# Kernel tuning notes

Measured on AMD Instinct MI355X. Metric: run time of the kernel, lower is better.

## Reference

```python
import jax, jax.numpy as jnp
import numpy as np

B, C, O, H, W, K, PAD = 8, 256, 256, 56, 56, 3, 1
KK = K * K


def setup_inputs() -> dict:
    key = jax.random.key(0)
    k1, k2, k3, k4 = jax.random.split(key, 4)
    x = jax.random.normal(k1, (B, C, H, W), jnp.float32)
    # offset conv params (original zero-inits; small random used so sampling is off-grid)
    w_off = jax.random.normal(k2, (2 * KK, C, K, K), jnp.float32) * 0.01
    b_off = jnp.zeros((2 * KK,), jnp.float32)
    # deformable conv weight/bias (torchvision DeformConv2d default has bias)
    w_dcn = jax.random.normal(k3, (O, C, K, K), jnp.float32) * (1.0 / np.sqrt(C * KK))
    b_dcn = jax.random.normal(k4, (O,), jnp.float32) * 0.01
    return dict(x=x, w_off=w_off, b_off=b_off, w_dcn=w_dcn, b_dcn=b_dcn)


def _conv3x3(x, w, b):
    y = jax.lax.conv_general_dilated(
        x, w, window_strides=(1, 1), padding=((PAD, PAD), (PAD, PAD)),
        dimension_numbers=('NCHW', 'OIHW', 'NCHW'))
    return y + b[None, :, None, None]


def _deform_sample(x, py, px):
    """Zero-padded bilinear gather of x[B,C,H,W] at (py,px)[B,KK,H,W] -> [B,C,KK,H,W]."""
    xf = x.reshape(B, C, H * W)
    y0 = jnp.floor(py)
    x0 = jnp.floor(px)
    fy = py - y0
    fx = px - x0
    val = 0.0
    for dy, dx, wgt in ((0, 0, (1 - fy) * (1 - fx)),
                        (0, 1, (1 - fy) * fx),
                        (1, 0, fy * (1 - fx)),
                        (1, 1, fy * fx)):
        yc = y0 + dy
        xc = x0 + dx
        ok = (yc >= 0) & (yc < H) & (xc >= 0) & (xc < W)  # zero-padding outside
        yi = jnp.clip(yc, 0, H - 1).astype(jnp.int32)
        xi = jnp.clip(xc, 0, W - 1).astype(jnp.int32)
        idx = (yi * W + xi).reshape(B, 1, KK * H * W)  # broadcast over channel dim
        g = jnp.take_along_axis(xf, idx, axis=2).reshape(B, C, KK, H, W)
        val = val + (wgt * ok)[:, None] * g
    return val


def reference(x, w_off, b_off, w_dcn, b_dcn):
    # 1) predict per-pixel offsets: [B, 2*K*K, H, W], torchvision layout (dy,dx) pairs
    off = _conv3x3(x, w_off, b_off)
    dy = off[:, 0::2]  # [B, KK, H, W]
    dx = off[:, 1::2]
    # 2) sampling grid: base pixel + kernel tap offset + learned offset
    ky = (jnp.arange(KK) // K - PAD).astype(jnp.float32)
    kx = (jnp.arange(KK) % K - PAD).astype(jnp.float32)
    hgrid = jnp.arange(H, dtype=jnp.float32)
    wgrid = jnp.arange(W, dtype=jnp.float32)
    py = hgrid[None, None, :, None] + ky[None, :, None, None] + dy
    px = wgrid[None, None, None, :] + kx[None, :, None, None] + dx
    # 3) bilinear gather + weighted accumulation over (c, kernel tap)
    val = _deform_sample(x, py, px)  # [B, C, KK, H, W]
    out = jnp.einsum('bckhw,ock->bohw', val, w_dcn.reshape(O, C, KK))
    return out + b_dcn[None, :, None, None]
```

## Files before the change

### kernel.cpp

```cpp
#include <hip/hip_runtime.h>

#define B_  8
#define C_  256
#define O_  256
#define H_  56
#define W_  56
#define HW_ 3136
#define KK_ 9
#define CK_ 2304
#define NKC 72

typedef __bf16    bf16x8 __attribute__((ext_vector_type(8)));
typedef float     f32x4  __attribute__((ext_vector_type(4)));

__device__ __forceinline__ void async16(const void* gsrc_lane, void* lds_uniform) {
    __builtin_amdgcn_global_load_lds(
        (const __attribute__((address_space(1))) unsigned int*)gsrc_lane,
        (__attribute__((address_space(3))) unsigned int*)lds_uniform, 16, 0, 0);
}

__device__ __forceinline__ int swz4(int r) { return (r & 3) ^ ((r >> 2) & 3); }

__device__ __forceinline__ float blo(unsigned u) {
    return __builtin_bit_cast(float, u << 16);
}
__device__ __forceinline__ float bhi(unsigned u) {
    return __builtin_bit_cast(float, u & 0xffff0000u);
}
__device__ __forceinline__ unsigned pkbf(float lo, float hi) {
    unsigned short a = __builtin_bit_cast(unsigned short, (__bf16)lo);
    unsigned short b = __builtin_bit_cast(unsigned short, (__bf16)hi);
    return (unsigned)a | ((unsigned)b << 16);
}

__device__ __forceinline__ uint4 bilin4(uint4 c00, uint4 c01, uint4 c10, uint4 c11,
                                        float4 wg) {
    uint4 o;
    float lo_, hi_;
    lo_ = wg.x*blo(c00.x) + wg.y*blo(c01.x) + wg.z*blo(c10.x) + wg.w*blo(c11.x);
    hi_ = wg.x*bhi(c00.x) + wg.y*bhi(c01.x) + wg.z*bhi(c10.x) + wg.w*bhi(c11.x);
    o.x = pkbf(lo_, hi_);
    lo_ = wg.x*blo(c00.y) + wg.y*blo(c01.y) + wg.z*blo(c10.y) + wg.w*blo(c11.y);
    hi_ = wg.x*bhi(c00.y) + wg.y*bhi(c01.y) + wg.z*bhi(c10.y) + wg.w*bhi(c11.y);
    o.y = pkbf(lo_, hi_);
    lo_ = wg.x*blo(c00.z) + wg.y*blo(c01.z) + wg.z*blo(c10.z) + wg.w*blo(c11.z);
    hi_ = wg.x*bhi(c00.z) + wg.y*bhi(c01.z) + wg.z*bhi(c10.z) + wg.w*bhi(c11.z);
    o.z = pkbf(lo_, hi_);
    lo_ = wg.x*blo(c00.w) + wg.y*blo(c01.w) + wg.z*blo(c10.w) + wg.w*blo(c11.w);
    hi_ = wg.x*bhi(c00.w) + wg.y*bhi(c01.w) + wg.z*bhi(c10.w) + wg.w*bhi(c11.w);
    o.w = pkbf(lo_, hi_);
    return o;
}

__global__ __launch_bounds__(256) void k_buildA(const float* __restrict__ w,
                                                unsigned short* __restrict__ wA) {
    int d  = blockIdx.x * 256 + threadIdx.x;
    int kc = d >> 13;
    int rd = d & 8191;
    int m  = rd >> 5;
    int pos = rd & 31;
    int q  = (pos >> 3) ^ swz4(m);
    int kl = q * 8 + (pos & 7);
    int gk = kc * 32 + kl;
    int tap = gk >> 8, c = gk & 255;
    __bf16 v = (__bf16)w[m * CK_ + c * KK_ + tap];
    wA[d] = __builtin_bit_cast(unsigned short, v);
}

__global__ __launch_bounds__(256) void k_transx(const float* __restrict__ x,
                                                unsigned short* __restrict__ xT) {
    __shared__ float s[64][65];
    int bt   = blockIdx.x;
    int c64  = bt & 3;
    int hw64 = (bt >> 2) % 49;
    int b    = bt / 196;
    int tx = threadIdx.x & 63;
    int ty = threadIdx.x >> 6;
#pragma unroll
    for (int i = 0; i < 16; ++i)
        s[i * 4 + ty][tx] =
            x[((size_t)(b * 256 + c64 * 64 + i * 4 + ty)) * HW_ + hw64 * 64 + tx];
    __syncthreads();
#pragma unroll
    for (int i = 0; i < 16; ++i) {
        float v = s[tx][i * 4 + ty];
        xT[((size_t)b * HW_ + hw64 * 64 + i * 4 + ty) * 256 + c64 * 64 + tx] =
            __builtin_bit_cast(unsigned short, (__bf16)v);
    }
}

__global__ __launch_bounds__(512) void k_offc1(const float* __restrict__ x,
                                               const float* __restrict__ w_off,
                                               float* __restrict__ part) {
    __shared__ float partial[8][64][18];
    int t  = threadIdx.x;
    int p  = t & 63;
    int cg = __builtin_amdgcn_readfirstlane(t >> 6);
    int blk  = blockIdx.x;
    int sl   = blk & 3;
    int un   = blk >> 2;
    int b    = un / 49;
    int pos0 = (un % 49) * 64;
    int pos  = pos0 + p;
    int h = pos / W_;
    int w = pos % W_;
    const float* xb = x + (size_t)b * C_ * HW_;

    float acc[18];
#pragma unroll
    for (int i = 0; i < 18; ++i) acc[i] = 0.f;

    for (int cc = 0; cc < 8; ++cc) {
        int c = sl * 64 + cg * 8 + cc;
        const float* xp = xb + c * HW_;
        float v[9];
#pragma unroll
        for (int dh = -1; dh <= 1; ++dh)
#pragma unroll
            for (int dw = -1; dw <= 1; ++dw) {
                int hh = h + dh, ww = w + dw;
                bool ok = (hh >= 0) & (hh < H_) & (ww >= 0) & (ww < W_);
                v[(dh + 1) * 3 + dw + 1] = ok ? xp[hh * W_ + ww] : 0.f;
            }
        const float* wc = w_off + c * KK_;
#pragma unroll
        for (int oc = 0; oc < 18; ++oc) {
            const float* wr = wc + oc * CK_;
#pragma unroll
            for (int k = 0; k < KK_; ++k)
                acc[oc] = fmaf(v[k], wr[k], acc[oc]);
        }
    }
#pragma unroll
    for (int oc = 0; oc < 18; ++oc) partial[cg][p][oc] = acc[oc];
    __syncthreads();

    float* po = part + (size_t)sl * (B_ * 18 * HW_);
    for (int e = t; e < 64 * 18; e += 512) {
        int oc = e >> 6;
        int pp = e & 63;
        float s = 0.f;
#pragma unroll
        for (int g = 0; g < 8; ++g) s += partial[g][pp][oc];
        po[((size_t)b * 18 + oc) * HW_ + pos0 + pp] = s;
    }
}

__global__ __launch_bounds__(256) void k_offc2(const float* __restrict__ part,
                                               const float* __restrict__ b_off,
                                               float* __restrict__ off) {
    int i = blockIdx.x * 256 + threadIdx.x;
    const int NP = B_ * 18 * HW_;
    int oc = (i / HW_) % 18;
    off[i] = part[i] + part[i + NP] + part[i + 2 * NP] + part[i + 3 * NP]
           + b_off[oc];
}

__device__ __forceinline__ void fstage(
    int s, int chNext, bool issueA, bool prod, bool reload,
    const char* xb, const char* gA0,
    __bf16 (*s_a)[8192], __bf16 (*s_b)[2048],
    int (*s_id)[64][4], float (*s_w)[64][4],
    int4& id, float4& wg,
    int n, int tc, int sc, int wv, int lid, int quad, int swz, int lo,
    f32x4 (&acc)[4][4]) {

    if (reload) {
        int tp1 = (s + 1) >> 3;
        id = *(const int4*)s_id[tp1][n];
        wg = *(const float4*)s_w[tp1][n];
    }
    uint4 c00, c01, c10, c11;
    if (prod) {
        const char* p = xb + chNext * 64 + tc * 16;
        c00 = *(const uint4*)(p + id.x);
        c01 = *(const uint4*)(p + id.y);
        c10 = *(const uint4*)(p + id.z);
        c11 = *(const uint4*)(p + id.w);
    }
    if (issueA) {
        const char* ga = gA0 + (size_t)(s + 2) * 16384;
        char* la = (char*)s_a[(s + 2) % 3];
#pragma unroll
        for (int j = 0; j < 4; ++j)
            async16(ga + wv * 4096 + j * 1024 + lo, la + wv * 4096 + j * 1024);
    }
    asm volatile("s_waitcnt vmcnt(12)" ::: "memory");

    const bf16x8* pa = (const bf16x8*)s_a[s % 3];
    const bf16x8* pb = (const bf16x8*)s_b[s & 1];
    bf16x8 af[4], bv[4];
#pragma unroll
    for (int mi = 0; mi < 4; ++mi)
        af[mi] = pa[(wv * 64 + mi * 16 + lid) * 4 + (quad ^ swz)];
#pragma unroll
    for (int ni = 0; ni < 4; ++ni)
        bv[ni] = pb[(ni * 16 + lid) * 4 + (quad ^ swz)];

    __builtin_amdgcn_s_setprio(1);
#pragma unroll
    for (int mi = 0; mi < 4; ++mi)
#pragma unroll
        for (int ni = 0; ni < 4; ++ni)
            acc[mi][ni] = __builtin_amdgcn_mfma_f32_16x16x32_bf16(
                af[mi], bv[ni], acc[mi][ni], 0, 0, 0);
    __builtin_amdgcn_s_setprio(0);

    if (prod) {
        uint4 o = bilin4(c00, c01, c10, c11, wg);
        *(uint4*)((char*)s_b[(s & 1) ^ 1] + n * 64 + sc * 16) = o;
    }
    asm volatile("s_waitcnt lgkmcnt(0)" ::: "memory");
    __builtin_amdgcn_s_barrier();
    __builtin_amdgcn_sched_barrier(0);
}

__global__ __launch_bounds__(256, 2) void k_fused(
    const unsigned short* __restrict__ xT,
    const float* __restrict__ off,
    const __bf16* __restrict__ wA,
    const float* __restrict__ b_dcn,
    float* __restrict__ out) {

    __shared__ __bf16 s_a[3][8192];
    __shared__ __bf16 s_b[2][2048];
    __shared__ int    s_id[KK_][64][4];
    __shared__ float  s_w [KK_][64][4];

    int g    = blockIdx.x;
    int b    = g / 49;
    int pos0 = (g % 49) * 64;
    int t    = threadIdx.x;
    int lane = t & 63;
    int wv   = t >> 6;
    int lid  = lane & 15;
    int quad = lane >> 4;
    int swz  = swz4(lid);

    for (int e = t; e < KK_ * 64; e += 256) {
        int k = e >> 6, n = e & 63;
        int pos = pos0 + n;
        int h = pos / W_, w = pos % W_;
        float dy = off[((size_t)b * 18 + 2 * k) * HW_ + pos];
        float dx = off[((size_t)b * 18 + 2 * k + 1) * HW_ + pos];
        float py = (float)(h + k / 3 - 1) + dy;
        float px = (float)(w + k % 3 - 1) + dx;
        float y0f = floorf(py), x0f = floorf(px);
        float fy = py - y0f, fx = px - x0f;
        int y0 = (int)y0f, x0 = (int)x0f;
        int y1 = y0 + 1,   x1 = x0 + 1;
        float oy0 = (y0 >= 0 && y0 < H_) ? 1.f : 0.f;
        float oy1 = (y1 >= 0 && y1 < H_) ? 1.f : 0.f;
        float ox0 = (x0 >= 0 && x0 < W_) ? 1.f : 0.f;
        float ox1 = (x1 >= 0 && x1 < W_) ? 1.f : 0.f;
        int y0c = min(max(y0, 0), H_ - 1), y1c = min(max(y1, 0), H_ - 1);
        int x0c = min(max(x0, 0), W_ - 1), x1c = min(max(x1, 0), W_ - 1);
        s_id[k][n][0] = (y0c * W_ + x0c) * 512;
        s_id[k][n][1] = (y0c * W_ + x1c) * 512;
        s_id[k][n][2] = (y1c * W_ + x0c) * 512;
        s_id[k][n][3] = (y1c * W_ + x1c) * 512;
        s_w[k][n][0] = (1.f - fy) * (1.f - fx) * oy0 * ox0;
        s_w[k][n][1] = (1.f - fy) * fx         * oy0 * ox1;
        s_w[k][n][2] = fy * (1.f - fx)         * oy1 * ox0;
        s_w[k][n][3] = fy * fx                 * oy1 * ox1;
    }
    __syncthreads();

    int n  = t >> 2;
    int tc = t & 3;
    int sc = tc ^ swz4(n);
    const char* xb  = (const char*)(xT + (size_t)b * HW_ * 256);
    const char* gA0 = (const char*)wA;
    int lo = lane * 16;

    f32x4 acc[4][4];
#pragma unroll
    for (int mi = 0; mi < 4; ++mi)
#pragma unroll
        for (int ni = 0; ni < 4; ++ni)
            acc[mi][ni] = (f32x4)(0.f);

    int4   id = *(const int4*)s_id[0][n];
    float4 wg = *(const float4*)s_w[0][n];
    {
        const char* p = xb + tc * 16;
        uint4 c00 = *(const uint4*)(p + id.x);
        uint4 c01 = *(const uint4*)(p + id.y);
        uint4 c10 = *(const uint4*)(p + id.z);
        uint4 c11 = *(const uint4*)(p + id.w);
#pragma unroll
        for (int ss = 0; ss < 2; ++ss) {
            const char* ga = gA0 + (size_t)ss * 16384;
            char* la = (char*)s_a[ss];
#pragma unroll
            for (int j = 0; j < 4; ++j)
                async16(ga + wv * 4096 + j * 1024 + lo, la + wv * 4096 + j * 1024);
        }
        uint4 o = bilin4(c00, c01, c10, c11, wg);
        *(uint4*)((char*)s_b[0] + n * 64 + sc * 16) = o;
    }
    asm volatile("s_waitcnt lgkmcnt(0)" ::: "memory");
    __builtin_amdgcn_s_barrier();
    __builtin_amdgcn_sched_barrier(0);

    for (int tap = 0; tap < 8; ++tap) {
        int s0 = tap * 8;
#pragma unroll
        for (int i = 0; i < 8; ++i)
            fstage(s0 + i, (i + 1) & 7, true, true, i == 7,
                   xb, gA0, s_a, s_b, s_id, s_w, id, wg,
                   n, tc, sc, wv, lid, quad, swz, lo, acc);
    }
#pragma unroll
    for (int i = 0; i < 8; ++i)
        fstage(64 + i, (i + 1) & 7, i < 6, i < 7, false,
               xb, gA0, s_a, s_b, s_id, s_w, id, wg,
               n, tc, sc, wv, lid, quad, swz, lo, acc);

#pragma unroll
    for (int mi = 0; mi < 4; ++mi) {
#pragma unroll
        for (int r = 0; r < 4; ++r) {
            int m = wv * 64 + mi * 16 + quad * 4 + r;
            float bias = b_dcn[m];
            float* po = out + ((size_t)b * O_ + m) * HW_ + pos0 + lid;
#pragma unroll
            for (int ni = 0; ni < 4; ++ni)
                po[ni * 16] = acc[mi][ni][r] + bias;
        }
    }
}

extern "C" void kernel_launch(void* const* d_in, const int* in_sizes, int n_in,
                              void* d_out, int out_size, void* d_ws, size_t ws_size,
                              hipStream_t stream) {
    const float* x     = (const float*)d_in[0];
    const float* w_off = (const float*)d_in[1];
    const float* b_off = (const float*)d_in[2];
    const float* w_dcn = (const float*)d_in[3];
    const float* b_dcn = (const float*)d_in[4];
    float* out = (float*)d_out;

    const size_t offBytes  = (size_t)451584 * 4;
    const size_t wABytes   = (size_t)589824 * 2;
    const size_t xTBytes   = (size_t)B_ * HW_ * 256 * 2;
    float*          off  = (float*)d_ws;
    unsigned short* wA   = (unsigned short*)((char*)d_ws + offBytes);
    unsigned short* xT   = (unsigned short*)((char*)d_ws + offBytes + wABytes);
    float*          part = (float*)((char*)d_ws + offBytes + wABytes + xTBytes);

    k_buildA <<<2304, 256, 0, stream>>>(w_dcn, wA);
    k_transx <<<1568, 256, 0, stream>>>(x, xT);
    k_offc1  <<<1568, 512, 0, stream>>>(x, w_off, part);
    k_offc2  <<<1764, 256, 0, stream>>>(part, b_off, off);
    k_fused  <<<392,  256, 0, stream>>>(xT, off, (const __bf16*)wA, b_dcn, out);
}
```

Before: 202.7 us.

## Halve fused DCN tile to 32 pixels, double-buffer A, raise occupancy, remap blocks

The fused deformable GEMM kernel now processes 32 output pixels per block instead of 64. This doubles the grid to 784 blocks and halves the B-tile and accumulator footprint. Weight staging drops from triple to double buffering with adjusted waitcnts, and launch bounds allow 3 blocks per CU. Block indices in the fused and offset-conv kernels are also remapped to interleave batches across XCDs. The aim is more parallelism and occupancy on 256 CUs, at the cost of re-streaming the weight matrix twice as often and a shallower prefetch.

```diff
diff --git a/kernel.cpp b/kernel.cpp
--- a/kernel.cpp
+++ b/kernel.cpp
@@ -33,9 +33,9 @@
     return (unsigned)a | ((unsigned)b << 16);
 }
 
-__device__ __forceinline__ uint4 bilin4(uint4 c00, uint4 c01, uint4 c10, uint4 c11,
+__device__ __forceinline__ uint2 bilin2(uint2 c00, uint2 c01, uint2 c10, uint2 c11,
                                         float4 wg) {
-    uint4 o;
+    uint2 o;
     float lo_, hi_;
     lo_ = wg.x*blo(c00.x) + wg.y*blo(c01.x) + wg.z*blo(c10.x) + wg.w*blo(c11.x);
     hi_ = wg.x*bhi(c00.x) + wg.y*bhi(c01.x) + wg.z*bhi(c10.x) + wg.w*bhi(c11.x);
@@ -43,12 +43,6 @@
     lo_ = wg.x*blo(c00.y) + wg.y*blo(c01.y) + wg.z*blo(c10.y) + wg.w*blo(c11.y);
     hi_ = wg.x*bhi(c00.y) + wg.y*bhi(c01.y) + wg.z*bhi(c10.y) + wg.w*bhi(c11.y);
     o.y = pkbf(lo_, hi_);
-    lo_ = wg.x*blo(c00.z) + wg.y*blo(c01.z) + wg.z*blo(c10.z) + wg.w*blo(c11.z);
-    hi_ = wg.x*bhi(c00.z) + wg.y*bhi(c01.z) + wg.z*bhi(c10.z) + wg.w*bhi(c11.z);
-    o.z = pkbf(lo_, hi_);
-    lo_ = wg.x*blo(c00.w) + wg.y*blo(c01.w) + wg.z*blo(c10.w) + wg.w*blo(c11.w);
-    hi_ = wg.x*bhi(c00.w) + wg.y*bhi(c01.w) + wg.z*bhi(c10.w) + wg.w*bhi(c11.w);
-    o.w = pkbf(lo_, hi_);
     return o;
 }
 
@@ -96,7 +90,8 @@
     int t  = threadIdx.x;
     int p  = t & 63;
     int cg = __builtin_amdgcn_readfirstlane(t >> 6);
-    int blk  = blockIdx.x;
+    int orig = blockIdx.x;
+    int blk  = (orig & 7) * 196 + (orig >> 3);
     int sl   = blk & 3;
     int un   = blk >> 2;
     int b    = un / 49;
@@ -157,79 +152,85 @@
 }
 
 __device__ __forceinline__ void fstage(
-    int s, int chNext, bool issueA, bool prod, bool reload,
+    int s, int chNext, bool issueA, bool prod, bool reload, bool last,
     const char* xb, const char* gA0,
-    __bf16 (*s_a)[8192], __bf16 (*s_b)[2048],
-    int (*s_id)[64][4], float (*s_w)[64][4],
+    __bf16 (*s_a)[8192], __bf16 (*s_b)[1024],
+    int (*s_id)[32][4], float (*s_w)[32][4],
     int4& id, float4& wg,
-    int n, int tc, int sc, int wv, int lid, int quad, int swz, int lo,
-    f32x4 (&acc)[4][4]) {
+    int n, int tc, int wrsc, int wv, int lid, int quad, int swz, int lo,
+    f32x4 (&acc)[4][2]) {
 
     if (reload) {
         int tp1 = (s + 1) >> 3;
         id = *(const int4*)s_id[tp1][n];
         wg = *(const float4*)s_w[tp1][n];
     }
-    uint4 c00, c01, c10, c11;
+    uint2 c00, c01, c10, c11;
     if (prod) {
-        const char* p = xb + chNext * 64 + tc * 16;
-        c00 = *(const uint4*)(p + id.x);
-        c01 = *(const uint4*)(p + id.y);
-        c10 = *(const uint4*)(p + id.z);
-        c11 = *(const uint4*)(p + id.w);
+        const char* p = xb + chNext * 64 + tc * 8;
+        c00 = *(const uint2*)(p + id.x);
+        c01 = *(const uint2*)(p + id.y);
+        c10 = *(const uint2*)(p + id.z);
+        c11 = *(const uint2*)(p + id.w);
     }
     if (issueA) {
-        const char* ga = gA0 + (size_t)(s + 2) * 16384;
-        char* la = (char*)s_a[(s + 2) % 3];
+        const char* ga = gA0 + (size_t)(s + 1) * 16384;
+        char* la = (char*)s_a[(s + 1) & 1];
 #pragma unroll
         for (int j = 0; j < 4; ++j)
             async16(ga + wv * 4096 + j * 1024 + lo, la + wv * 4096 + j * 1024);
     }
-    asm volatile("s_waitcnt vmcnt(12)" ::: "memory");
-
-    const bf16x8* pa = (const bf16x8*)s_a[s % 3];
+    if (last) {
+        asm volatile("s_waitcnt vmcnt(0)" ::: "memory");
+    } else {
+        asm volatile("s_waitcnt vmcnt(8)" ::: "memory");
+    }
+
+    const bf16x8* pa = (const bf16x8*)s_a[s & 1];
     const bf16x8* pb = (const bf16x8*)s_b[s & 1];
-    bf16x8 af[4], bv[4];
+    bf16x8 af[4], bv[2];
 #pragma unroll
     for (int mi = 0; mi < 4; ++mi)
         af[mi] = pa[(wv * 64 + mi * 16 + lid) * 4 + (quad ^ swz)];
 #pragma unroll
-    for (int ni = 0; ni < 4; ++ni)
+    for (int ni = 0; ni < 2; ++ni)
         bv[ni] = pb[(ni * 16 + lid) * 4 + (quad ^ swz)];
 
     __builtin_amdgcn_s_setprio(1);
 #pragma unroll
     for (int mi = 0; mi < 4; ++mi)
 #pragma unroll
-        for (int ni = 0; ni < 4; ++ni)
+        for (int ni = 0; ni < 2; ++ni)
             acc[mi][ni] = __builtin_amdgcn_mfma_f32_16x16x32_bf16(
                 af[mi], bv[ni], acc[mi][ni], 0, 0, 0);
     __builtin_amdgcn_s_setprio(0);
+    __builtin_amdgcn_sched_barrier(0);
 
     if (prod) {
-        uint4 o = bilin4(c00, c01, c10, c11, wg);
-        *(uint4*)((char*)s_b[(s & 1) ^ 1] + n * 64 + sc * 16) = o;
+        uint2 o = bilin2(c00, c01, c10, c11, wg);
+        *(uint2*)((char*)s_b[(s & 1) ^ 1] + wrsc) = o;
     }
     asm volatile("s_waitcnt lgkmcnt(0)" ::: "memory");
     __builtin_amdgcn_s_barrier();
     __builtin_amdgcn_sched_barrier(0);
 }
 
-__global__ __launch_bounds__(256, 2) void k_fused(
+__global__ __launch_bounds__(256, 3) void k_fused(
     const unsigned short* __restrict__ xT,
     const float* __restrict__ off,
     const __bf16* __restrict__ wA,
     const float* __restrict__ b_dcn,
     float* __restrict__ out) {
 
-    __shared__ __bf16 s_a[3][8192];
-    __shared__ __bf16 s_b[2][2048];
-    __shared__ int    s_id[KK_][64][4];
-    __shared__ float  s_w [KK_][64][4];
-
-    int g    = blockIdx.x;
-    int b    = g / 49;
-    int pos0 = (g % 49) * 64;
+    __shared__ __bf16 s_a[2][8192];
+    __shared__ __bf16 s_b[2][1024];
+    __shared__ int    s_id[KK_][32][4];
+    __shared__ float  s_w [KK_][32][4];
+
+    int bid  = blockIdx.x;
+    int u    = (bid & 7) * 98 + (bid >> 3);
+    int b    = u / 98;
+    int pos0 = (u % 98) * 32;
     int t    = threadIdx.x;
     int lane = t & 63;
     int wv   = t >> 6;
@@ -237,8 +238,8 @@
     int quad = lane >> 4;
     int swz  = swz4(lid);
 
-    for (int e = t; e < KK_ * 64; e += 256) {
-        int k = e >> 6, n = e & 63;
+    for (int e = t; e < KK_ * 32; e += 256) {
+        int k = e >> 5, n = e & 31;
         int pos = pos0 + n;
         int h = pos / W_, w = pos % W_;
         float dy = off[((size_t)b * 18 + 2 * k) * HW_ + pos];
@@ -266,38 +267,34 @@
     }
     __syncthreads();
 
-    int n  = t >> 2;
-    int tc = t & 3;
-    int sc = tc ^ swz4(n);
+    int n  = t >> 3;
+    int tc = t & 7;
+    int wrsc = n * 64 + (((tc >> 1) ^ swz4(n)) << 4) + (tc & 1) * 8;
     const char* xb  = (const char*)(xT + (size_t)b * HW_ * 256);
     const char* gA0 = (const char*)wA;
     int lo = lane * 16;
 
-    f32x4 acc[4][4];
+    f32x4 acc[4][2];
 #pragma unroll
     for (int mi = 0; mi < 4; ++mi)
 #pragma unroll
-        for (int ni = 0; ni < 4; ++ni)
+        for (int ni = 0; ni < 2; ++ni)
             acc[mi][ni] = (f32x4)(0.f);
 
     int4   id = *(const int4*)s_id[0][n];
     float4 wg = *(const float4*)s_w[0][n];
     {
-        const char* p = xb + tc * 16;
-        uint4 c00 = *(const uint4*)(p + id.x);
-        uint4 c01 = *(const uint4*)(p + id.y);
-        uint4 c10 = *(const uint4*)(p + id.z);
-        uint4 c11 = *(const uint4*)(p + id.w);
-#pragma unroll
-        for (int ss = 0; ss < 2; ++ss) {
-            const char* ga = gA0 + (size_t)ss * 16384;
-            char* la = (char*)s_a[ss];
-#pragma unroll
-            for (int j = 0; j < 4; ++j)
-                async16(ga + wv * 4096 + j * 1024 + lo, la + wv * 4096 + j * 1024);
-        }
-        uint4 o = bilin4(c00, c01, c10, c11, wg);
-        *(uint4*)((char*)s_b[0] + n * 64 + sc * 16) = o;
+        const char* p = xb + tc * 8;
+        uint2 c00 = *(const uint2*)(p + id.x);
+        uint2 c01 = *(const uint2*)(p + id.y);
+        uint2 c10 = *(const uint2*)(p + id.z);
+        uint2 c11 = *(const uint2*)(p + id.w);
+#pragma unroll
+        for (int j = 0; j < 4; ++j)
+            async16(gA0 + wv * 4096 + j * 1024 + lo,
+                    (char*)s_a[0] + wv * 4096 + j * 1024);
+        uint2 o = bilin2(c00, c01, c10, c11, wg);
+        *(uint2*)((char*)s_b[0] + wrsc) = o;
     }
     asm volatile("s_waitcnt lgkmcnt(0)" ::: "memory");
     __builtin_amdgcn_s_barrier();
@@ -307,15 +304,15 @@
         int s0 = tap * 8;
 #pragma unroll
         for (int i = 0; i < 8; ++i)
-            fstage(s0 + i, (i + 1) & 7, true, true, i == 7,
+            fstage(s0 + i, (i + 1) & 7, true, true, i == 7, false,
                    xb, gA0, s_a, s_b, s_id, s_w, id, wg,
-                   n, tc, sc, wv, lid, quad, swz, lo, acc);
+                   n, tc, wrsc, wv, lid, quad, swz, lo, acc);
     }
 #pragma unroll
     for (int i = 0; i < 8; ++i)
-        fstage(64 + i, (i + 1) & 7, i < 6, i < 7, false,
+        fstage(64 + i, (i + 1) & 7, i < 7, i < 7, false, i == 7,
                xb, gA0, s_a, s_b, s_id, s_w, id, wg,
-               n, tc, sc, wv, lid, quad, swz, lo, acc);
+               n, tc, wrsc, wv, lid, quad, swz, lo, acc);
 
 #pragma unroll
     for (int mi = 0; mi < 4; ++mi) {
@@ -325,7 +322,7 @@
             float bias = b_dcn[m];
             float* po = out + ((size_t)b * O_ + m) * HW_ + pos0 + lid;
 #pragma unroll
-            for (int ni = 0; ni < 4; ++ni)
+            for (int ni = 0; ni < 2; ++ni)
                 po[ni * 16] = acc[mi][ni][r] + bias;
         }
     }
@@ -353,5 +350,5 @@
     k_transx <<<1568, 256, 0, stream>>>(x, xT);
     k_offc1  <<<1568, 512, 0, stream>>>(x, w_off, part);
     k_offc2  <<<1764, 256, 0, stream>>>(part, b_off, off);
-    k_fused  <<<392,  256, 0, stream>>>(xT, off, (const __bf16*)wA, b_dcn, out);
-}
+    k_fused  <<<784,  256, 0, stream>>>(xT, off, (const __bf16*)wA, b_dcn, out);
+}
```

After: 241.3 us. 19.0% more time.
